# Performance work log

Hardware: AMD Instinct MI355X
Metric: run time of the kernel (lower is better)

Reference implementation:

```python
import jax, jax.numpy as jnp
import numpy as np

BSZ = 32768
K = 4096  # 1 positive + (K-1) negatives

def setup_inputs() -> dict:
    key = jax.random.key(0)
    x = jax.random.normal(key, (BSZ, K), dtype=jnp.float32)
    # ~mean CE for random logits is log(K)~8.3 -> mask keeps roughly half the samples
    threshold = jnp.float32(8.3)
    return {"x": x, "threshold": threshold}

def reference(x, threshold):
    # per-sample cross-entropy vs label 0: -log_softmax(x)[:, 0]
    loss = jax.nn.logsumexp(x, axis=1) - x[:, 0]          # [BSZ]
    mask = (loss > threshold).astype(loss.dtype)          # [BSZ]
    count = mask.sum()
    loss_t = (loss * mask).sum()
    # if no element exceeds threshold: count=1, loss_t=loss[0]
    return jnp.where(count == 0, loss[0], loss_t / jnp.maximum(count, 1.0))
```

## Files before the change

### kernel.cpp

```cpp
#include <hip/hip_runtime.h>
#include <math.h>

#define K_DIM 4096
#define BSZ 32768
#define BLOCK 256
#define WAVES_PER_BLOCK (BLOCK / 64)
#define ROWS_PER_WAVE 4
#define GRID (BSZ / (WAVES_PER_BLOCK * ROWS_PER_WAVE))

typedef float f32x4 __attribute__((ext_vector_type(4)));

__global__ __launch_bounds__(BLOCK) void row_loss_kernel(
    const float* __restrict__ x, float* __restrict__ loss_out) {
  const int t = threadIdx.x;
  const int lane = t & 63;
  const int gw = blockIdx.x * WAVES_PER_BLOCK + (t >> 6);

  const f32x4* x4 = reinterpret_cast<const f32x4*>(x);

#pragma unroll
  for (int r = 0; r < ROWS_PER_WAVE; ++r) {
    const int row = gw * ROWS_PER_WAVE + r;
    const f32x4* xr = x4 + (size_t)row * (K_DIM / 4);

    f32x4 v[16];
#pragma unroll
    for (int i = 0; i < 16; ++i) {
      v[i] = __builtin_nontemporal_load(xr + i * 64 + lane);
    }
    asm volatile(""
                 : "+v"(v[0]), "+v"(v[1]), "+v"(v[2]), "+v"(v[3]),
                   "+v"(v[4]), "+v"(v[5]), "+v"(v[6]), "+v"(v[7]),
                   "+v"(v[8]), "+v"(v[9]), "+v"(v[10]), "+v"(v[11]),
                   "+v"(v[12]), "+v"(v[13]), "+v"(v[14]), "+v"(v[15]));

    const float x0 = v[0].x;

    float s = 0.f;
#pragma unroll
    for (int i = 0; i < 16; ++i) {
      s += __expf(v[i].x) + __expf(v[i].y) + __expf(v[i].z) + __expf(v[i].w);
    }
#pragma unroll
    for (int off = 32; off >= 1; off >>= 1) s += __shfl_xor(s, off);

    if (lane == 0) loss_out[row] = __logf(s) - x0;
  }
}

__global__ __launch_bounds__(1024) void finalize_kernel(
    const float* __restrict__ loss, const float* __restrict__ thr_p,
    float* __restrict__ out) {
  __shared__ float s_sum[1024 / 64];
  __shared__ float s_cnt[1024 / 64];

  const float thr = *thr_p;
  const int t = threadIdx.x;
  const f32x4* l4 = reinterpret_cast<const f32x4*>(loss);

  float sum = 0.f, cnt = 0.f;
#pragma unroll
  for (int i = 0; i < BSZ / 4 / 1024; ++i) {
    f32x4 v = l4[i * 1024 + t];
#pragma unroll
    for (int j = 0; j < 4; ++j) {
      if (v[j] > thr) { sum += v[j]; cnt += 1.f; }
    }
  }
#pragma unroll
  for (int off = 32; off >= 1; off >>= 1) {
    sum += __shfl_xor(sum, off);
    cnt += __shfl_xor(cnt, off);
  }
  const int wave = t >> 6;
  const int lane = t & 63;
  if (lane == 0) { s_sum[wave] = sum; s_cnt[wave] = cnt; }
  __syncthreads();
  if (t == 0) {
    float S = 0.f, C = 0.f;
#pragma unroll
    for (int w = 0; w < 1024 / 64; ++w) { S += s_sum[w]; C += s_cnt[w]; }
    out[0] = (C == 0.f) ? loss[0] : S / fmaxf(C, 1.f);
  }
}

extern "C" void kernel_launch(void* const* d_in, const int* in_sizes, int n_in,
                              void* d_out, int out_size, void* d_ws,
                              size_t ws_size, hipStream_t stream) {
  const float* x = (const float*)d_in[0];
  const float* thr = (const float*)d_in[1];
  float* out = (float*)d_out;
  float* loss = (float*)d_ws;

  row_loss_kernel<<<GRID, BLOCK, 0, stream>>>(x, loss);
  finalize_kernel<<<1, 1024, 0, stream>>>(loss, thr, out);
}
```

Before: 89.13 us.

## Fuse finalize into row-loss kernel via atomics and last-block ticket

Merges the per-row loss kernel and the single-block finalize kernel into one launch. Each block reduces its masked sum and count, adds them atomically to a global accumulator, and the last block to increment a ticket counter writes the final mean. This removes the per-row loss buffer round trip and the second launch, but adds a memset launch, global float atomics whose summation order is nondeterministic, and a relaxed-order dependency for the row-0 fallback value.

Result: slower. 182.9 us (+105.2%).

```diff
diff --git a/kernel.cpp b/kernel.cpp
--- a/kernel.cpp
+++ b/kernel.cpp
@@ -10,13 +10,19 @@
 
 typedef float f32x4 __attribute__((ext_vector_type(4)));
 
-__global__ __launch_bounds__(BLOCK) void row_loss_kernel(
-    const float* __restrict__ x, float* __restrict__ loss_out) {
+__global__ __launch_bounds__(BLOCK) void fused_kernel(
+    const float* __restrict__ x, const float* __restrict__ thr_p,
+    float* __restrict__ out, float* __restrict__ acc,
+    unsigned* __restrict__ ticket) {
   const int t = threadIdx.x;
   const int lane = t & 63;
-  const int gw = blockIdx.x * WAVES_PER_BLOCK + (t >> 6);
+  const int w = t >> 6;
+  const int gw = blockIdx.x * WAVES_PER_BLOCK + w;
 
+  const float thr = *thr_p;
   const f32x4* x4 = reinterpret_cast<const f32x4*>(x);
+
+  float wsum = 0.f, wcnt = 0.f;
 
 #pragma unroll
   for (int r = 0; r < ROWS_PER_WAVE; ++r) {
@@ -44,43 +50,44 @@
 #pragma unroll
     for (int off = 32; off >= 1; off >>= 1) s += __shfl_xor(s, off);
 
-    if (lane == 0) loss_out[row] = __logf(s) - x0;
-  }
-}
-
-__global__ __launch_bounds__(1024) void finalize_kernel(
-    const float* __restrict__ loss, const float* __restrict__ thr_p,
-    float* __restrict__ out) {
-  __shared__ float s_sum[1024 / 64];
-  __shared__ float s_cnt[1024 / 64];
-
-  const float thr = *thr_p;
-  const int t = threadIdx.x;
-  const f32x4* l4 = reinterpret_cast<const f32x4*>(loss);
-
-  float sum = 0.f, cnt = 0.f;
-#pragma unroll
-  for (int i = 0; i < BSZ / 4 / 1024; ++i) {
-    f32x4 v = l4[i * 1024 + t];
-#pragma unroll
-    for (int j = 0; j < 4; ++j) {
-      if (v[j] > thr) { sum += v[j]; cnt += 1.f; }
+    if (lane == 0) {
+      const float l = __logf(s) - x0;
+      if (row == 0) {
+        __hip_atomic_store(&acc[2], l, __ATOMIC_RELAXED,
+                           __HIP_MEMORY_SCOPE_AGENT);
+      }
+      if (l > thr) {
+        wsum += l;
+        wcnt += 1.f;
+      }
     }
   }
-#pragma unroll
-  for (int off = 32; off >= 1; off >>= 1) {
-    sum += __shfl_xor(sum, off);
-    cnt += __shfl_xor(cnt, off);
+
+  __shared__ float bs[WAVES_PER_BLOCK];
+  __shared__ float bc[WAVES_PER_BLOCK];
+  if (lane == 0) {
+    bs[w] = wsum;
+    bc[w] = wcnt;
   }
-  const int wave = t >> 6;
-  const int lane = t & 63;
-  if (lane == 0) { s_sum[wave] = sum; s_cnt[wave] = cnt; }
   __syncthreads();
   if (t == 0) {
-    float S = 0.f, C = 0.f;
-#pragma unroll
-    for (int w = 0; w < 1024 / 64; ++w) { S += s_sum[w]; C += s_cnt[w]; }
-    out[0] = (C == 0.f) ? loss[0] : S / fmaxf(C, 1.f);
+    const float S = (bs[0] + bs[1]) + (bs[2] + bs[3]);
+    const float C = (bc[0] + bc[1]) + (bc[2] + bc[3]);
+    if (C > 0.f) {
+      atomicAdd(&acc[0], S);
+      atomicAdd(&acc[1], C);
+    }
+    const unsigned old = __hip_atomic_fetch_add(ticket, 1u, __ATOMIC_ACQ_REL,
+                                                __HIP_MEMORY_SCOPE_AGENT);
+    if (old == GRID - 1) {
+      const float sum =
+          __hip_atomic_load(&acc[0], __ATOMIC_RELAXED, __HIP_MEMORY_SCOPE_AGENT);
+      const float cnt =
+          __hip_atomic_load(&acc[1], __ATOMIC_RELAXED, __HIP_MEMORY_SCOPE_AGENT);
+      const float l0 =
+          __hip_atomic_load(&acc[2], __ATOMIC_RELAXED, __HIP_MEMORY_SCOPE_AGENT);
+      out[0] = (cnt == 0.f) ? l0 : sum / fmaxf(cnt, 1.f);
+    }
   }
 }
 
@@ -90,8 +97,9 @@
   const float* x = (const float*)d_in[0];
   const float* thr = (const float*)d_in[1];
   float* out = (float*)d_out;
-  float* loss = (float*)d_ws;
+  float* acc = (float*)d_ws;
+  unsigned* ticket = (unsigned*)(acc + 3);
 
-  row_loss_kernel<<<GRID, BLOCK, 0, stream>>>(x, loss);
-  finalize_kernel<<<1, 1024, 0, stream>>>(loss, thr, out);
+  hipMemsetAsync(d_ws, 0, 16, stream);
+  fused_kernel<<<GRID, BLOCK, 0, stream>>>(x, thr, out, acc, ticket);
 }
```
